# Kernel optimization log

Hardware: AMD Instinct MI355X
Metric: run time of the kernel (lower is better)

Reference implementation:

```python
import jax, jax.numpy as jnp
import numpy as np

B, S, D, VOCAB, K = 32, 128, 300, 20000, 8


def setup_inputs() -> dict:
    key = jax.random.key(0)
    ks = jax.random.split(key, 12)
    return {
        "words": jax.random.normal(ks[0], (B, S, D), jnp.float32),
        "lengths": jax.random.randint(ks[1], (B,), S // 2, S + 1),
        "vocab": jax.random.normal(ks[2], (VOCAB, D), jnp.float32) * 0.1,
        "default_embed": jax.random.uniform(ks[3], (D,), jnp.float32),
        "W": jnp.eye(D, dtype=jnp.float32) + 0.01 * jax.random.normal(ks[4], (D, D), jnp.float32),
        "lstm_Wih": jax.random.normal(ks[5], (4 * D, D), jnp.float32) * 0.05,
        "lstm_Whh": jax.random.normal(ks[6], (4 * D, D), jnp.float32) * 0.05,
        "lstm_bih": jnp.zeros((4 * D,), jnp.float32),
        "lstm_bhh": jnp.zeros((4 * D,), jnp.float32),
        "rnn_Wih": jax.random.normal(ks[7], (D, D), jnp.float32) * 0.05,
        "rnn_Whh": jax.random.normal(ks[8], (D, D), jnp.float32) * 0.05,
        "rnn_bih": jnp.zeros((D,), jnp.float32),
        "rnn_bhh": jnp.zeros((D,), jnp.float32),
    }


def _forward(words, lengths, vocab, default_embed, W,
             lstm_Wih, lstm_Whh, lstm_bih, lstm_bhh,
             rnn_Wih, rnn_Whh, rnn_bih, rnn_bhh):
    b, s, d = words.shape
    # --- NormalizeWordsModel (tagger) ---
    C = jnp.concatenate([vocab.T, default_embed[:, None]], axis=1)  # [D, V+1]
    P = jax.nn.softmax(jnp.einsum("bsd,de,ev->bsv", words, W, C), axis=-1)  # [B,S,V+1]
    V = P[..., -1:] * words + jnp.einsum("bsv,vd->bsd", P[..., :-1], vocab)  # [B,S,D]

    # --- LSTM encoder, final hidden at true length (packed-sequence semantics) ---
    valid = (jnp.arange(s)[None, :] < lengths[:, None])  # [B,S]

    def lstm_step(carry, xs):
        h, c = carry
        x_t, v_t = xs  # [B,D], [B]
        gates = x_t @ lstm_Wih.T + lstm_bih + h @ lstm_Whh.T + lstm_bhh  # [B,4D]
        i, f, g, o = jnp.split(gates, 4, axis=-1)
        c_new = jax.nn.sigmoid(f) * c + jax.nn.sigmoid(i) * jnp.tanh(g)
        h_new = jax.nn.sigmoid(o) * jnp.tanh(c_new)
        m = v_t[:, None]
        h = jnp.where(m, h_new, h)
        c = jnp.where(m, c_new, c)
        return (h, c), None

    h0 = jnp.zeros((b, d), V.dtype)
    (q, _), _ = jax.lax.scan(lstm_step, (h0, h0),
                             (jnp.swapaxes(V, 0, 1), valid.T))  # q: [B,D]

    # --- InstructionsDecoder: RNNCell applied K times to the same input q ---
    def rnn_step(h, _):
        h2 = jnp.tanh(q @ rnn_Wih.T + rnn_bih + h @ rnn_Whh.T + rnn_bhh)
        return h2, h2

    _, H = jax.lax.scan(rnn_step, h0, None, length=K)  # [K,B,D]
    H = jnp.swapaxes(H, 0, 1)  # [B,K,D]

    # --- masked softmax attention readout ---
    scores = jnp.einsum("bkd,bsd->bks", H, V)  # [B,K,S]
    scores = jnp.where(valid[:, None, :], scores, -jnp.inf)
    R = jnp.einsum("bks,bsd->bkd", jax.nn.softmax(scores, axis=-1), V)
    return R


def reference(words, lengths, vocab, default_embed, W,
              lstm_Wih, lstm_Whh, lstm_bih, lstm_bhh,
              rnn_Wih, rnn_Whh, rnn_bih, rnn_bhh):
    return _forward(words, lengths, vocab, default_embed, W,
                    lstm_Wih, lstm_Whh, lstm_bih, lstm_bhh,
                    rnn_Wih, rnn_Whh, rnn_bih, rnn_bhh)
```

## Files before the change

kernel.cpp:

```cpp
#include <hip/hip_runtime.h>


typedef unsigned short u16;
typedef unsigned int   u32;
typedef float  f32x4 __attribute__((ext_vector_type(4)));
typedef u32    u32x4 __attribute__((ext_vector_type(4)));
typedef __bf16 bf16x8 __attribute__((ext_vector_type(8)));
typedef _Float16 f16x2 __attribute__((ext_vector_type(2)));
typedef _Float16 f16x8 __attribute__((ext_vector_type(8)));

#define SCOPE_AGENT __HIP_MEMORY_SCOPE_AGENT

__device__ __forceinline__ float bf2f(u16 u) { return __uint_as_float(((u32)u) << 16); }
__device__ __forceinline__ u16 f2bf(float f) {
  u32 x = __float_as_uint(f);
  u32 r = (x + 0x7fffu + ((x >> 16) & 1u)) >> 16;
  return (u16)r;
}
__device__ __forceinline__ float sigm(float x) { return 1.f / (1.f + __expf(-x)); }
__device__ __forceinline__ u16 f2h(float f) {
  union { _Float16 h; u16 u; } cv; cv.h = (_Float16)f; return cv.u;
}
__device__ __forceinline__ float h2f(u16 u) {
  union { _Float16 h; u16 u; } cv; cv.u = u; return (float)cv.h;
}

__device__ __forceinline__ f32x4 shflx4(f32x4 v, int m) {
  f32x4 r;
  r[0] = __shfl_xor(v[0], m, 16);
  r[1] = __shfl_xor(v[1], m, 16);
  r[2] = __shfl_xor(v[2], m, 16);
  r[3] = __shfl_xor(v[3], m, 16);
  return r;
}

__device__ __forceinline__ void conv_seg(const void* src, u16* dst, int n, int is32,
                                         int t0, int stride) {
  if (is32) {
    const float* s = (const float*)src;
    for (int i = t0; i < n; i += stride) dst[i] = f2bf(s[i]);
  } else {
    const u16* s = (const u16*)src;
    for (int i = t0; i < n; i += stride) dst[i] = s[i];
  }
}

__global__ __launch_bounds__(256) void k_ingest(
    const void* words, const void* vocab, const void* de, const void* W,
    const void* lWih, const void* lWhh, const void* lbih, const void* lbhh,
    const void* rWih, const void* rWhh, const void* rbih, const void* rbhh,
    u16* cw, u16* cv, u16* cde, u16* cW, u16* cWih, u16* cWhh, u16* cbih, u16* cbhh,
    u16* crWih, u16* crWhh, u16* crbih, u16* crbhh, u32* flag, u32* seqz, u32* hbz) {
  __shared__ int s_is32;
  int tid = threadIdx.x;
  int vote = 0;
  if (tid < 64) {
    u32 w = ((const u32*)words)[tid];
    int e = (w >> 7) & 0xFF;
    vote = (e >= 100 && e <= 150) ? 1 : 0;
  }
  unsigned long long m = __ballot(vote);
  if (tid == 0) s_is32 = (__popcll(m) < 32) ? 1 : 0;
  __syncthreads();
  int is32 = s_is32;
  if (blockIdx.x == 0 && tid == 0) *flag = (u32)is32;
  int t0 = blockIdx.x * 256 + tid;
  int stride = gridDim.x * 256;
  if (t0 < 256) seqz[t0] = 0;
  if (t0 < 10240) hbz[t0] = 0;
  conv_seg(words, cw, 1228800, is32, t0, stride);
  conv_seg(vocab, cv, 6000000, is32, t0, stride);
  conv_seg(de, cde, 300, is32, t0, stride);
  conv_seg(W, cW, 90000, is32, t0, stride);
  conv_seg(lWih, cWih, 360000, is32, t0, stride);
  conv_seg(lWhh, cWhh, 360000, is32, t0, stride);
  conv_seg(lbih, cbih, 1200, is32, t0, stride);
  conv_seg(lbhh, cbhh, 1200, is32, t0, stride);
  conv_seg(rWih, crWih, 90000, is32, t0, stride);
  conv_seg(rWhh, crWhh, 90000, is32, t0, stride);
  conv_seg(rbih, crbih, 300, is32, t0, stride);
  conv_seg(rbhh, crbhh, 300, is32, t0, stride);
}

__global__ __launch_bounds__(256) void k_transpose_bf(const u16* __restrict__ in,
                                                      u16* __restrict__ out,
                                                      int J, int K) {
  __shared__ u16 t[32][33];
  int j0 = blockIdx.x * 32, k0 = blockIdx.y * 32;
  int lx = threadIdx.x & 31, ly = threadIdx.x >> 5;
  for (int r = ly; r < 32; r += 8) {
    int j = j0 + r, k = k0 + lx;
    t[r][lx] = (j < J && k < K) ? in[(size_t)j * K + k] : (u16)0;
  }
  __syncthreads();
  for (int r = ly; r < 32; r += 8) {
    int k = k0 + r, j = j0 + lx;
    if (k < K && j < J) out[(size_t)k * J + j] = t[lx][r];
  }
}

__global__ __launch_bounds__(256) void k_pack_w4(const u16* __restrict__ Whh,
                                                 u16* __restrict__ pW) {
  int idx = blockIdx.x * 256 + threadIdx.x;
  if (idx >= 16 * 25600) return;
  int bid = idx / 25600, r = idx % 25600;
  int t2 = r >> 9, lane = (r >> 3) & 63, j = r & 7;
  int nt = t2 / 10, kt = t2 % 10;
  int n = nt * 16 + (lane & 15);
  int gate = n / 20, dl = n % 20;
  int d0 = (bid < 15) ? 19 * bid : 285;
  int nd = (bid < 15) ? 19 : 15;
  int k = kt * 32 + ((lane >> 4) * 8) + j;
  u16 out = 0;
  if (dl < nd && k < 300) out = f2h(bf2f(Whh[(size_t)(gate * 300 + d0 + dl) * 300 + k]));
  pW[idx] = out;
}

__global__ __launch_bounds__(256) void k_pack_vocab(const u16* __restrict__ vocab,
                                                    u16* __restrict__ pA,
                                                    u16* __restrict__ pB) {
  __shared__ u16 sv[32][320];
  int ci = blockIdx.x, tid = threadIdx.x;
  for (int idx = tid; idx < 32 * 20; idx += 256) {
    int v = idx / 20, k = 300 + (idx - v * 20);
    sv[v][k] = 0;
  }
  for (int idx = tid; idx < 32 * 300; idx += 256) {
    int v = idx / 300, k = idx - v * 300;
    sv[v][k] = vocab[(size_t)(ci * 32 + v) * 300 + k];
  }
  __syncthreads();
  for (int idx = tid; idx < 10240; idx += 256) {
    int j = idx & 7, lane = (idx >> 3) & 63, t2 = idx >> 9;
    int kk = t2 % 10, h = t2 / 10;
    int v = h * 16 + (lane & 15);
    int k = kk * 32 + ((lane >> 4)) * 8 + j;
    pA[(size_t)ci * 10240 + (size_t)idx] = sv[v][k];
  }
  for (int idx = tid; idx < 9728; idx += 256) {
    int j = idx & 7, lane = (idx >> 3) & 63, nc = idx >> 9;
    int v = (lane >> 4) * 8 + j;
    int n = nc * 16 + (lane & 15);
    pB[(size_t)ci * 9728 + (size_t)idx] = sv[v][n];
  }
}

__global__ __launch_bounds__(256) void k_xw(const u16* __restrict__ words,
                                            const u16* __restrict__ W,
                                            u16* __restrict__ X) {
  __shared__ float As[300][33];
  int n0 = blockIdx.x * 128;
  int r0 = blockIdx.y * 32;
  int tid = threadIdx.x;
  for (int idx = tid; idx < 32 * 300; idx += 256) {
    int r = idx / 300, k = idx - r * 300;
    As[k][r] = bf2f(words[(size_t)(r0 + r) * 300 + k]);
  }
  __syncthreads();
  int j = n0 + (tid & 127);
  int rh = (tid >> 7) * 16;
  float acc[16];
#pragma unroll
  for (int i = 0; i < 16; i++) acc[i] = 0.f;
  if (j < 300) {
    for (int k = 0; k < 300; k++) {
      float bw = bf2f(W[(size_t)k * 300 + j]);
#pragma unroll
      for (int i = 0; i < 16; i++) acc[i] += As[k][rh + i] * bw;
    }
  }
  if (j < 320) {
#pragma unroll
    for (int i = 0; i < 16; i++) {
      float v = (j < 300) ? acc[i] : 0.f;
      X[(size_t)(r0 + rh + i) * 320 + j] = f2bf(v);
    }
  }
}

__global__ __launch_bounds__(512, 2) void k_softmax_v(
    const u16* __restrict__ X, const u16* __restrict__ pA, const u16* __restrict__ pB,
    u16* __restrict__ pAcc, float* __restrict__ pML) {
  __shared__ __align__(16) u16 chunk[19968];
  __shared__ __align__(16) float ptbuf[8 * 576];
  int bid = blockIdx.x;
  int sl = bid & 7, b = bid >> 3;
  int tid = threadIdx.x;
  int w = tid >> 6, lane = tid & 63;
  int quad = lane >> 4, n16 = lane & 15;
  int cs = (sl == 0) ? 0 : 79 + (sl - 1) * 78;
  int nch = (sl == 0) ? 79 : 78;

  int rowA = b * 128 + w * 16 + n16;
  const bf16x8* Xrow = (const bf16x8*)(X + (size_t)rowA * 320);
  bf16x8 afr[10];
#pragma unroll
  for (int kk = 0; kk < 10; kk++) afr[kk] = Xrow[kk * 4 + quad];

  f32x4 acc[19];
#pragma unroll
  for (int i = 0; i < 19; i++) { acc[i][0] = 0.f; acc[i][1] = 0.f; acc[i][2] = 0.f; acc[i][3] = 0.f; }
  f32x4 mrun, lrun;
#pragma unroll
  for (int c = 0; c < 4; c++) { mrun[c] = -1e30f; lrun[c] = 0.f; }
  float* myPt = ptbuf + w * 576;

  {
    const u32x4* gA = (const u32x4*)pA + (size_t)cs * 1280;
    const u32x4* gB = (const u32x4*)pB + (size_t)cs * 1216;
    u32x4* sb = (u32x4*)&chunk[0];
    for (int idx = tid; idx < 2496; idx += 512)
      sb[idx] = (idx < 1280) ? gA[idx] : gB[idx - 1280];
  }
  __syncthreads();

  for (int ic = 0; ic < nch; ic++) {
    u32x4 pf[5];
    bool havepf = (ic + 1 < nch);
    if (havepf) {
      int ci = cs + ic + 1;
      const u32x4* gA = (const u32x4*)pA + (size_t)ci * 1280;
      const u32x4* gB = (const u32x4*)pB + (size_t)ci * 1216;
#pragma unroll
      for (int i = 0; i < 5; i++) {
        int idx = tid + i * 512;
        if (idx < 2496) pf[i] = (idx < 1280) ? gA[idx] : gB[idx - 1280];
      }
    }
    const bf16x8* bufA = (const bf16x8*)&chunk[0];
    const bf16x8* bufB = (const bf16x8*)&chunk[10240];
    f32x4 L0, L1;
#pragma unroll
    for (int c = 0; c < 4; c++) { L0[c] = 0.f; L1[c] = 0.f; }
#pragma unroll
    for (int kk = 0; kk < 10; kk++) {
      L0 = __builtin_amdgcn_mfma_f32_16x16x32_bf16(afr[kk], bufA[kk * 64 + lane], L0, 0, 0, 0);
      L1 = __builtin_amdgcn_mfma_f32_16x16x32_bf16(afr[kk], bufA[(10 + kk) * 64 + lane], L1, 0, 0, 0);
    }
    f32x4 t;
#pragma unroll
    for (int c = 0; c < 4; c++) t[c] = fmaxf(L0[c], L1[c]);
#pragma unroll
    for (int off = 1; off < 16; off <<= 1) {
      f32x4 o = shflx4(t, off);
#pragma unroll
      for (int c = 0; c < 4; c++) t[c] = fmaxf(t[c], o[c]);
    }
    f32x4 mnew, al, P0v, P1v, rs;
#pragma unroll
    for (int c = 0; c < 4; c++) {
      mnew[c] = fmaxf(mrun[c], t[c]);
      al[c] = __expf(mrun[c] - mnew[c]);
      P0v[c] = __expf(L0[c] - mnew[c]);
      P1v[c] = __expf(L1[c] - mnew[c]);
      rs[c] = P0v[c] + P1v[c];
    }
#pragma unroll
    for (int off = 1; off < 16; off <<= 1) {
      f32x4 o = shflx4(rs, off);
#pragma unroll
      for (int c = 0; c < 4; c++) rs[c] += o[c];
    }
#pragma unroll
    for (int c = 0; c < 4; c++) { lrun[c] = lrun[c] * al[c] + rs[c]; mrun[c] = mnew[c]; }
#pragma unroll
    for (int r = 0; r < 4; r++) {
      myPt[(quad * 4 + r) * 36 + n16] = P0v[r];
      myPt[(quad * 4 + r) * 36 + 16 + n16] = P1v[r];
    }
    __syncthreads();
    f32x4 plo = *(const f32x4*)(myPt + n16 * 36 + quad * 8);
    f32x4 phi = *(const f32x4*)(myPt + n16 * 36 + quad * 8 + 4);
    bf16x8 paf;
#pragma unroll
    for (int c = 0; c < 4; c++) { paf[c] = (__bf16)plo[c]; paf[c + 4] = (__bf16)phi[c]; }
#pragma unroll
    for (int nc = 0; nc < 19; nc++) {
      f32x4 a = acc[nc];
#pragma unroll
      for (int c = 0; c < 4; c++) a[c] *= al[c];
      acc[nc] = __builtin_amdgcn_mfma_f32_16x16x32_bf16(paf, bufB[nc * 64 + lane], a, 0, 0, 0);
    }
    __syncthreads();
    if (havepf) {
      u32x4* sb = (u32x4*)&chunk[0];
#pragma unroll
      for (int i = 0; i < 5; i++) {
        int idx = tid + i * 512;
        if (idx < 2496) sb[idx] = pf[i];
      }
    }
    __syncthreads();
  }

  size_t prow = (size_t)sl * 4096 + (size_t)b * 128 + w * 16;
  if (n16 == 0) {
#pragma unroll
    for (int r = 0; r < 4; r++) {
      pML[(prow + quad * 4 + r) * 2 + 0] = mrun[r];
      pML[(prow + quad * 4 + r) * 2 + 1] = lrun[r];
    }
  }
#pragma unroll
  for (int nc = 0; nc < 19; nc++)
#pragma unroll
    for (int r = 0; r < 4; r++)
      pAcc[(prow + quad * 4 + r) * 304 + nc * 16 + n16] = f2bf(acc[nc][r]);
}

__global__ __launch_bounds__(320) void k_combine(
    const u16* __restrict__ pAcc, const float* __restrict__ pML,
    const u16* __restrict__ X, const u16* __restrict__ de,
    const u16* __restrict__ words, u16* __restrict__ Vout) {
  __shared__ float red[320];
  __shared__ float fs[8];
  __shared__ float sinv, sw;
  int row = blockIdx.x, tid = threadIdx.x;
  float p = 0.f;
  if (tid < 300) p = bf2f(X[(size_t)row * 320 + tid]) * bf2f(de[tid]);
  red[tid] = p;
  __syncthreads();
  if (tid == 0) {
    float d = 0.f;
    for (int i = 0; i < 300; i++) d += red[i];
    float mv[8], lv[8], ms = -1e30f;
    for (int s = 0; s < 8; s++) {
      mv[s] = pML[((size_t)s * 4096 + row) * 2];
      lv[s] = pML[((size_t)s * 4096 + row) * 2 + 1];
      ms = fmaxf(ms, mv[s]);
    }
    float mf = fmaxf(ms, d);
    float pd = __expf(d - mf);
    float l = pd;
    for (int s = 0; s < 8; s++) {
      float f = __expf(mv[s] - mf);
      fs[s] = f;
      l += lv[s] * f;
    }
    sinv = 1.f / l;
    sw = pd / l;
  }
  __syncthreads();
  float v = 0.f;
  if (tid < 300) {
    float a = 0.f;
#pragma unroll
    for (int s = 0; s < 8; s++)
      a += bf2f(pAcc[((size_t)s * 4096 + row) * 304 + tid]) * fs[s];
    v = a * sinv + sw * bf2f(words[(size_t)row * 300 + tid]);
  }
  Vout[(size_t)row * 320 + tid] = f2bf(v);
}

__global__ __launch_bounds__(256) void k_xg(const u16* __restrict__ Vb,
                                            const u16* __restrict__ WihT,
                                            const u16* __restrict__ bih,
                                            const u16* __restrict__ bhh,
                                            float* __restrict__ xg) {
  __shared__ float As[300][33];
  int n0 = blockIdx.x * 128;
  int r0 = blockIdx.y * 32;
  int tid = threadIdx.x;
  for (int idx = tid; idx < 32 * 300; idx += 256) {
    int r = idx / 300, k = idx - r * 300;
    As[k][r] = bf2f(Vb[(size_t)(r0 + r) * 320 + k]);
  }
  __syncthreads();
  int j = n0 + (tid & 127);
  if (j >= 1200) return;
  int rh = (tid >> 7) * 16;
  float acc[16];
#pragma unroll
  for (int i = 0; i < 16; i++) acc[i] = 0.f;
  for (int k = 0; k < 300; k++) {
    float bw = bf2f(WihT[(size_t)k * 1200 + j]);
#pragma unroll
    for (int i = 0; i < 16; i++) acc[i] += As[k][rh + i] * bw;
  }
  float bias = bf2f(bih[j]) + bf2f(bhh[j]);
#pragma unroll
  for (int i = 0; i < 16; i++)
    xg[(size_t)(r0 + rh + i) * 1200 + j] = acc[i] + bias;
}

__global__ __launch_bounds__(320, 1) void k_lstm2(
    const float* __restrict__ xg, const u16* __restrict__ pW,
    const int* __restrict__ lengths, u16* __restrict__ hb, u32* __restrict__ seq) {
  __shared__ float gl[32][84];
  __shared__ int s_maxlen;
  int bid = blockIdx.x, tid = threadIdx.x;
  int w = tid >> 6, lane = tid & 63;
  int quad = lane >> 4, n16 = lane & 15;
  int d0 = (bid < 15) ? 19 * bid : 285;
  int nd = (bid < 15) ? 19 : 15;
  {
    int lv = (tid < 32) ? lengths[tid] : 0;
    for (int off2 = 1; off2 < 32; off2 <<= 1) {
      int o = __shfl_xor(lv, off2, 64);
      lv = lv > o ? lv : o;
    }
    if (tid == 0) s_maxlen = lv;
  }
  f16x8 bf[10];
  const u32x4* pw4 = (const u32x4*)(pW + (size_t)bid * 25600);
#pragma unroll
  for (int kt = 0; kt < 10; kt++)
    bf[kt] = __builtin_bit_cast(f16x8, pw4[(w * 10 + kt) * 64 + lane]);
  int b0 = tid / 20, dl0 = tid - b0 * 20;
  int b1 = (tid + 320) / 20, dl1 = (tid + 320) - b1 * 20;
  bool a0 = dl0 < nd, a1 = dl1 < nd;
  int len0 = lengths[b0], len1 = lengths[b1];
  int dim0 = d0 + dl0, dim1 = d0 + dl1;
  int sa0 = (((b0 >> 4) * 10 + (dim0 >> 5)) * 64 + ((dim0 >> 3) & 3) * 16 + (b0 & 15)) * 8 + (dim0 & 7);
  int sa1 = (((b1 >> 4) * 10 + (dim1 >> 5)) * 64 + ((dim1 >> 3) & 3) * 16 + (b1 & 15)) * 8 + (dim1 & 7);
  float c0 = 0.f, h0 = 0.f, c1 = 0.f, h1 = 0.f;
  __syncthreads();
  int maxlen = s_maxlen;
  for (int t = 0; t < maxlen; t++) {
    if (tid < 16) {
      while (__hip_atomic_load(&seq[tid * 16], __ATOMIC_ACQUIRE, SCOPE_AGENT) < (u32)t)
        __builtin_amdgcn_s_sleep(2);
    }
    __syncthreads();
    float xv00 = 0.f, xv01 = 0.f, xv02 = 0.f, xv03 = 0.f;
    float xv10 = 0.f, xv11 = 0.f, xv12 = 0.f, xv13 = 0.f;
    const float* xr0 = xg + ((size_t)b0 * 128 + t) * 1200 + dim0;
    const float* xr1 = xg + ((size_t)b1 * 128 + t) * 1200 + dim1;
    if (a0) { xv00 = xr0[0]; xv01 = xr0[300]; xv02 = xr0[600]; xv03 = xr0[900]; }
    if (a1) { xv10 = xr1[0]; xv11 = xr1[300]; xv12 = xr1[600]; xv13 = xr1[900]; }
    const u32x4* hbt = (const u32x4*)hb + (size_t)(t & 1) * 1280;
    u32x4 af[2][10];
#pragma unroll
    for (int mt = 0; mt < 2; mt++)
#pragma unroll
      for (int kt = 0; kt < 10; kt++)
        af[mt][kt] = hbt[(mt * 10 + kt) * 64 + lane];
#pragma unroll
    for (int mt = 0; mt < 2; mt++) {
      f32x4 C;
      C[0] = 0.f; C[1] = 0.f; C[2] = 0.f; C[3] = 0.f;
#pragma unroll
      for (int kt = 0; kt < 10; kt++)
        C = __builtin_amdgcn_mfma_f32_16x16x32_f16(
            __builtin_bit_cast(f16x8, af[mt][kt]), bf[kt], C, 0, 0, 0);
#pragma unroll
      for (int rr = 0; rr < 4; rr++)
        gl[mt * 16 + quad * 4 + rr][w * 16 + n16] = C[rr];
    }
    __syncthreads();
    u16* hbw = hb + (size_t)((t + 1) & 1) * 10240;
    if (a0) {
      float gi = gl[b0][dl0] + xv00, gf = gl[b0][20 + dl0] + xv01;
      float gg = gl[b0][40 + dl0] + xv02, go = gl[b0][60 + dl0] + xv03;
      if (t < len0) {
        c0 = sigm(gf) * c0 + sigm(gi) * tanhf(gg);
        h0 = sigm(go) * tanhf(c0);
      }
      hbw[sa0] = f2h(h0);
    }
    if (a1) {
      float gi = gl[b1][dl1] + xv10, gf = gl[b1][20 + dl1] + xv11;
      float gg = gl[b1][40 + dl1] + xv12, go = gl[b1][60 + dl1] + xv13;
      if (t < len1) {
        c1 = sigm(gf) * c1 + sigm(gi) * tanhf(gg);
        h1 = sigm(go) * tanhf(c1);
      }
      hbw[sa1] = f2h(h1);
    }
    __syncthreads();
    if (tid == 0)
      __hip_atomic_store(&seq[bid * 16], (u32)(t + 1), __ATOMIC_RELEASE, SCOPE_AGENT);
  }
}

__global__ __launch_bounds__(320) void k_rnn(
    const u16* __restrict__ hb, const int* __restrict__ lengths,
    const u16* __restrict__ rWihT, const u16* __restrict__ rWhhT,
    const u16* __restrict__ rbih, const u16* __restrict__ rbhh,
    float* __restrict__ H) {
  __shared__ float qs[304], h2[304], base[304];
  __shared__ int s_maxlen;
  int b = blockIdx.x, tid = threadIdx.x;
  {
    int lv = (tid < 32) ? lengths[tid] : 0;
    for (int off2 = 1; off2 < 32; off2 <<= 1) {
      int o = __shfl_xor(lv, off2, 64);
      lv = lv > o ? lv : o;
    }
    if (tid == 0) s_maxlen = lv;
  }
  __syncthreads();
  int buf = s_maxlen & 1;
  if (tid < 304) {
    float q = 0.f;
    if (tid < 300) {
      int dim = tid;
      int idx = (((b >> 4) * 10 + (dim >> 5)) * 64 + ((dim >> 3) & 3) * 16 + (b & 15)) * 8 + (dim & 7);
      q = h2f(hb[(size_t)buf * 10240 + idx]);
    }
    qs[tid] = q;
    h2[tid] = 0.f;
  }
  __syncthreads();
  if (tid < 300) {
    float a = bf2f(rbih[tid]) + bf2f(rbhh[tid]);
    for (int k = 0; k < 300; k++) a += qs[k] * bf2f(rWihT[(size_t)k * 300 + tid]);
    base[tid] = a;
  }
  __syncthreads();
  for (int s = 0; s < 8; s++) {
    float nv = 0.f;
    if (tid < 300) {
      float a = base[tid];
      for (int k = 0; k < 300; k++) a += h2[k] * bf2f(rWhhT[(size_t)k * 300 + tid]);
      nv = tanhf(a);
    }
    __syncthreads();
    if (tid < 300) {
      h2[tid] = nv;
      H[((size_t)b * 8 + s) * 300 + tid] = nv;
    }
    __syncthreads();
  }
}

__global__ __launch_bounds__(256) void k_attn(const float* __restrict__ H,
                                              const u16* __restrict__ Vb,
                                              const int* __restrict__ lengths,
                                              const u32* __restrict__ flag,
                                              void* __restrict__ dout) {
  __shared__ float Hs[8][304];
  __shared__ float sc[8][128];
  __shared__ float wsum[8];
  int b = blockIdx.x, tid = threadIdx.x;
  int len = lengths[b];
  int is32 = (int)*flag;
  for (int idx = tid; idx < 8 * 300; idx += 256) {
    int k = idx / 300, j = idx - k * 300;
    Hs[k][j] = H[((size_t)b * 8 + k) * 300 + j];
  }
  __syncthreads();
  for (int s = tid; s < len; s += 256) {
    const u16* vr = Vb + (size_t)(b * 128 + s) * 320;
    float a[8];
#pragma unroll
    for (int k = 0; k < 8; k++) a[k] = 0.f;
    for (int j = 0; j < 300; j++) {
      float v = bf2f(vr[j]);
#pragma unroll
      for (int k = 0; k < 8; k++) a[k] += Hs[k][j] * v;
    }
#pragma unroll
    for (int k = 0; k < 8; k++) sc[k][s] = a[k];
  }
  __syncthreads();
  if (tid < 8) {
    float m = -1e30f;
    for (int s = 0; s < len; s++) m = fmaxf(m, sc[tid][s]);
    float l = 0.f;
    for (int s = 0; s < len; s++) { float e = __expf(sc[tid][s] - m); sc[tid][s] = e; l += e; }
    wsum[tid] = 1.f / l;
  }
  __syncthreads();
  int k = tid >> 5, jl = tid & 31;
  for (int j = jl; j < 300; j += 32) {
    float a = 0.f;
    for (int s = 0; s < len; s++) a += sc[k][s] * bf2f(Vb[(size_t)(b * 128 + s) * 320 + j]);
    float val = a * wsum[k];
    size_t o = ((size_t)b * 8 + k) * 300 + j;
    if (is32) ((float*)dout)[o] = val;
    else ((u16*)dout)[o] = f2bf(val);
  }
}

extern "C" void kernel_launch(void* const* d_in, const int* in_sizes, int n_in,
                              void* d_out, int out_size, void* d_ws, size_t ws_size,
                              hipStream_t stream) {
  (void)in_sizes; (void)n_in; (void)out_size; (void)ws_size;
  const void* words = d_in[0];
  const int* lengths = (const int*)d_in[1];
  const void* vocab = d_in[2];
  const void* de = d_in[3];
  const void* W = d_in[4];
  const void* lWih = d_in[5];
  const void* lWhh = d_in[6];
  const void* lbih = d_in[7];
  const void* lbhh = d_in[8];
  const void* rWih = d_in[9];
  const void* rWhh = d_in[10];
  const void* rbih = d_in[11];
  const void* rbhh = d_in[12];

  char* basep = (char*)d_ws;
  size_t off = 0;
  auto take = [&](size_t bytes) -> char* {
    char* p = basep + off;
    off += (bytes + 255) & ~(size_t)255;
    return p;
  };
  u16* cw    = (u16*)take(1228800 * 2);
  u16* cv    = (u16*)take(6000000 * 2);
  u16* cde   = (u16*)take(300 * 2);
  u16* cW    = (u16*)take(90000 * 2);
  u16* cWih  = (u16*)take(360000 * 2);
  u16* cWhh  = (u16*)take(360000 * 2);
  u16* cbih  = (u16*)take(1200 * 2);
  u16* cbhh  = (u16*)take(1200 * 2);
  u16* crWih = (u16*)take(90000 * 2);
  u16* crWhh = (u16*)take(90000 * 2);
  u16* crbih = (u16*)take(300 * 2);
  u16* crbhh = (u16*)take(300 * 2);
  u32* flag  = (u32*)take(256);
  u16*   X     = (u16*)take((size_t)4096 * 320 * 2);
  u16*   Vb    = (u16*)take((size_t)4096 * 320 * 2);
  u16*   WihT  = (u16*)take((size_t)300 * 1200 * 2);
  u16*   pW4   = (u16*)take((size_t)16 * 25600 * 2);
  u16*   rWihT = (u16*)take((size_t)300 * 300 * 2);
  u16*   rWhhT = (u16*)take((size_t)300 * 300 * 2);
  u16*   pAcc  = (u16*)take((size_t)8 * 4096 * 304 * 2);
  float* pML   = (float*)take((size_t)8 * 4096 * 2 * 4);
  float* H     = (float*)take((size_t)32 * 8 * 300 * 4);
  u16*   hb    = (u16*)take((size_t)2 * 10240 * 2);
  u32*   seq   = (u32*)take((size_t)4096 * 4);
  char* ureg = take((size_t)25000192);
  u16*   pA = (u16*)ureg;
  u16*   pB = (u16*)(ureg + (size_t)625 * 10240 * 2);
  float* xg = (float*)ureg;

  k_ingest<<<4096, 256, 0, stream>>>(words, vocab, de, W, lWih, lWhh, lbih, lbhh,
                                     rWih, rWhh, rbih, rbhh,
                                     cw, cv, cde, cW, cWih, cWhh, cbih, cbhh,
                                     crWih, crWhh, crbih, crbhh, flag, seq, (u32*)hb);
  k_transpose_bf<<<dim3(38, 10), 256, 0, stream>>>(cWih, WihT, 1200, 300);
  k_transpose_bf<<<dim3(10, 10), 256, 0, stream>>>(crWih, rWihT, 300, 300);
  k_transpose_bf<<<dim3(10, 10), 256, 0, stream>>>(crWhh, rWhhT, 300, 300);
  k_pack_w4<<<1600, 256, 0, stream>>>(cWhh, pW4);
  k_pack_vocab<<<625, 256, 0, stream>>>(cv, pA, pB);
  k_xw<<<dim3(3, 128), 256, 0, stream>>>(cw, cW, X);
  k_softmax_v<<<256, 512, 0, stream>>>(X, pA, pB, pAcc, pML);
  k_combine<<<4096, 320, 0, stream>>>(pAcc, pML, X, cde, cw, Vb);
  k_xg<<<dim3(10, 128), 256, 0, stream>>>(Vb, WihT, cbih, cbhh, xg);
  k_lstm2<<<16, 320, 0, stream>>>(xg, pW4, lengths, hb, seq);
  k_rnn<<<32, 320, 0, stream>>>(hb, lengths, rWihT, rWhhT, crbih, crbhh, H);
  k_attn<<<32, 256, 0, stream>>>(H, Vb, lengths, flag, d_out);
}
```

Before: 1.082 ms.

## Restructure LSTM recurrence into 19 single-wave blocks with register-resident weights

Replaces the 16-block, 320-thread LSTM kernel with 19 active single-wavefront blocks. Each block owns 16 hidden dims across all four gates and keeps its Whh fragments in registers. The gate math is done directly from MFMA accumulators, which removes the shared-memory gate staging and the per-step __syncthreads barriers. The input projection is now written as fp16 in a lane-packed layout, so each lane loads its step's inputs with four vector loads, and a new pad kernel zeroes the unused tail. The risks are lower precision for the input gates, busy-spin flag polling without sleep, and launching 152 blocks of which only every eighth does work, presumably to spread the active ones across CUs.

```diff
diff --git a/kernel.cpp b/kernel.cpp
--- a/kernel.cpp
+++ b/kernel.cpp
@@ -66,8 +66,8 @@
   if (blockIdx.x == 0 && tid == 0) *flag = (u32)is32;
   int t0 = blockIdx.x * 256 + tid;
   int stride = gridDim.x * 256;
-  if (t0 < 256) seqz[t0] = 0;
-  if (t0 < 10240) hbz[t0] = 0;
+  if (t0 < 608) seqz[t0] = 0;
+  if (t0 < 40960) hbz[t0] = 0;
   conv_seg(words, cw, 1228800, is32, t0, stride);
   conv_seg(vocab, cv, 6000000, is32, t0, stride);
   conv_seg(de, cde, 300, is32, t0, stride);
@@ -99,21 +99,19 @@
   }
 }
 
-__global__ __launch_bounds__(256) void k_pack_w4(const u16* __restrict__ Whh,
-                                                 u16* __restrict__ pW) {
+__global__ __launch_bounds__(256) void k_pack_wA(const u16* __restrict__ Whh,
+                                                 u16* __restrict__ pWn) {
   int idx = blockIdx.x * 256 + threadIdx.x;
-  if (idx >= 16 * 25600) return;
-  int bid = idx / 25600, r = idx % 25600;
-  int t2 = r >> 9, lane = (r >> 3) & 63, j = r & 7;
-  int nt = t2 / 10, kt = t2 % 10;
-  int n = nt * 16 + (lane & 15);
-  int gate = n / 20, dl = n % 20;
-  int d0 = (bid < 15) ? 19 * bid : 285;
-  int nd = (bid < 15) ? 19 : 15;
+  if (idx >= 389120) return;
+  int j = idx & 7, lane = (idx >> 3) & 63;
+  int t2 = idx >> 9;
+  int kt = t2 % 10, gw = t2 / 10;
+  int gate = gw & 3, wid = gw >> 2;
+  int dim = wid * 16 + (lane & 15);
   int k = kt * 32 + ((lane >> 4) * 8) + j;
   u16 out = 0;
-  if (dl < nd && k < 300) out = f2h(bf2f(Whh[(size_t)(gate * 300 + d0 + dl) * 300 + k]));
-  pW[idx] = out;
+  if (dim < 300 && k < 300) out = f2h(bf2f(Whh[(size_t)(gate * 300 + dim) * 300 + k]));
+  pWn[idx] = out;
 }
 
 __global__ __launch_bounds__(256) void k_pack_vocab(const u16* __restrict__ vocab,
@@ -352,11 +350,18 @@
   Vout[(size_t)row * 320 + tid] = f2bf(v);
 }
 
+__global__ __launch_bounds__(256) void k_xgp_pad(u32* __restrict__ xgp) {
+  int i = blockIdx.x * 256 + threadIdx.x;
+  if (i >= 32768) return;
+  int t = i >> 8, lane = 48 + ((i >> 4) & 15), d = i & 15;
+  xgp[((size_t)(t * 19 + 18) * 64 + lane) * 16 + d] = 0;
+}
+
 __global__ __launch_bounds__(256) void k_xg(const u16* __restrict__ Vb,
                                             const u16* __restrict__ WihT,
                                             const u16* __restrict__ bih,
                                             const u16* __restrict__ bhh,
-                                            float* __restrict__ xg) {
+                                            u16* __restrict__ xgp) {
   __shared__ float As[300][33];
   int n0 = blockIdx.x * 128;
   int r0 = blockIdx.y * 32;
@@ -378,98 +383,101 @@
     for (int i = 0; i < 16; i++) acc[i] += As[k][rh + i] * bw;
   }
   float bias = bf2f(bih[j]) + bf2f(bhh[j]);
-#pragma unroll
-  for (int i = 0; i < 16; i++)
-    xg[(size_t)(r0 + rh + i) * 1200 + j] = acc[i] + bias;
-}
-
-__global__ __launch_bounds__(320, 1) void k_lstm2(
-    const float* __restrict__ xg, const u16* __restrict__ pW,
+  int gate = j / 300, dim = j - gate * 300;
+  int wid = dim >> 4, dl = dim & 15;
+  int qd = dl >> 2, reg = dl & 3, rp = reg >> 1, half = reg & 1;
+  int b = r0 >> 7;
+  int tb = (r0 & 127) + rh;
+  size_t lanepart = (size_t)(qd * 16 + (b & 15)) * 16 + (b >> 4) * 8 + gate * 2 + rp;
+#pragma unroll
+  for (int i = 0; i < 16; i++) {
+    size_t u32idx = ((size_t)((tb + i) * 19 + wid) * 64) * 16 + lanepart;
+    xgp[u32idx * 2 + half] = f2h(acc[i] + bias);
+  }
+}
+
+__global__ __launch_bounds__(64, 1) void k_lstm3(
+    const u16* __restrict__ xgp, const u16* __restrict__ pWn,
     const int* __restrict__ lengths, u16* __restrict__ hb, u32* __restrict__ seq) {
-  __shared__ float gl[32][84];
-  __shared__ int s_maxlen;
-  int bid = blockIdx.x, tid = threadIdx.x;
-  int w = tid >> 6, lane = tid & 63;
+  int bid = blockIdx.x;
+  if (bid & 7) return;
+  int wid = bid >> 3;
+  if (wid >= 19) return;
+  int lane = threadIdx.x;
   int quad = lane >> 4, n16 = lane & 15;
-  int d0 = (bid < 15) ? 19 * bid : 285;
-  int nd = (bid < 15) ? 19 : 15;
-  {
-    int lv = (tid < 32) ? lengths[tid] : 0;
-    for (int off2 = 1; off2 < 32; off2 <<= 1) {
-      int o = __shfl_xor(lv, off2, 64);
-      lv = lv > o ? lv : o;
-    }
-    if (tid == 0) s_maxlen = lv;
-  }
-  f16x8 bf[10];
-  const u32x4* pw4 = (const u32x4*)(pW + (size_t)bid * 25600);
-#pragma unroll
-  for (int kt = 0; kt < 10; kt++)
-    bf[kt] = __builtin_bit_cast(f16x8, pw4[(w * 10 + kt) * 64 + lane]);
-  int b0 = tid / 20, dl0 = tid - b0 * 20;
-  int b1 = (tid + 320) / 20, dl1 = (tid + 320) - b1 * 20;
-  bool a0 = dl0 < nd, a1 = dl1 < nd;
-  int len0 = lengths[b0], len1 = lengths[b1];
-  int dim0 = d0 + dl0, dim1 = d0 + dl1;
-  int sa0 = (((b0 >> 4) * 10 + (dim0 >> 5)) * 64 + ((dim0 >> 3) & 3) * 16 + (b0 & 15)) * 8 + (dim0 & 7);
-  int sa1 = (((b1 >> 4) * 10 + (dim1 >> 5)) * 64 + ((dim1 >> 3) & 3) * 16 + (b1 & 15)) * 8 + (dim1 & 7);
-  float c0 = 0.f, h0 = 0.f, c1 = 0.f, h1 = 0.f;
-  __syncthreads();
-  int maxlen = s_maxlen;
+  int lv = (lane < 32) ? lengths[lane] : 0;
+#pragma unroll
+  for (int o = 1; o < 64; o <<= 1) {
+    int x = __shfl_xor(lv, o, 64);
+    lv = lv > x ? lv : x;
+  }
+  int maxlen = lv;
+  int len0 = lengths[n16], len1 = lengths[16 + n16];
+  u32x4 afr[4][10];
+  const u32x4* pw = (const u32x4*)pWn + (size_t)wid * 40 * 64;
+#pragma unroll
+  for (int g = 0; g < 4; g++)
+#pragma unroll
+    for (int kt = 0; kt < 10; kt++)
+      afr[g][kt] = pw[(g * 10 + kt) * 64 + lane];
+  float cst[2][4], hst[2][4];
+#pragma unroll
+  for (int mt = 0; mt < 2; mt++)
+#pragma unroll
+    for (int r = 0; r < 4; r++) { cst[mt][r] = 0.f; hst[mt][r] = 0.f; }
+
   for (int t = 0; t < maxlen; t++) {
-    if (tid < 16) {
-      while (__hip_atomic_load(&seq[tid * 16], __ATOMIC_ACQUIRE, SCOPE_AGENT) < (u32)t)
-        __builtin_amdgcn_s_sleep(2);
-    }
-    __syncthreads();
-    float xv00 = 0.f, xv01 = 0.f, xv02 = 0.f, xv03 = 0.f;
-    float xv10 = 0.f, xv11 = 0.f, xv12 = 0.f, xv13 = 0.f;
-    const float* xr0 = xg + ((size_t)b0 * 128 + t) * 1200 + dim0;
-    const float* xr1 = xg + ((size_t)b1 * 128 + t) * 1200 + dim1;
-    if (a0) { xv00 = xr0[0]; xv01 = xr0[300]; xv02 = xr0[600]; xv03 = xr0[900]; }
-    if (a1) { xv10 = xr1[0]; xv11 = xr1[300]; xv12 = xr1[600]; xv13 = xr1[900]; }
-    const u32x4* hbt = (const u32x4*)hb + (size_t)(t & 1) * 1280;
-    u32x4 af[2][10];
-#pragma unroll
-    for (int mt = 0; mt < 2; mt++)
+    u32 Xd[16];
+    {
+      const u32x4* xb = (const u32x4*)xgp + ((size_t)(t * 19 + wid) * 64 + lane) * 4;
+      *(u32x4*)&Xd[0] = xb[0];
+      *(u32x4*)&Xd[4] = xb[1];
+      *(u32x4*)&Xd[8] = xb[2];
+      *(u32x4*)&Xd[12] = xb[3];
+    }
+    if (lane < 19) {
+      while (__hip_atomic_load(&seq[lane * 32], __ATOMIC_ACQUIRE, SCOPE_AGENT) < (u32)t) {}
+    }
+    int rbuf = t & 1, wbuf = rbuf ^ 1;
+    const u16* hbr = hb + (size_t)rbuf * 40960;
+#pragma unroll
+    for (int mt = 0; mt < 2; mt++) {
+      int batch = mt * 16 + n16;
+      const u16* hbase = hbr + batch * 1280 + (quad & 1) * 8;
+      u32x4 bfr[10];
 #pragma unroll
       for (int kt = 0; kt < 10; kt++)
-        af[mt][kt] = hbt[(mt * 10 + kt) * 64 + lane];
-#pragma unroll
-    for (int mt = 0; mt < 2; mt++) {
-      f32x4 C;
-      C[0] = 0.f; C[1] = 0.f; C[2] = 0.f; C[3] = 0.f;
+        bfr[kt] = *(const u32x4*)(hbase + (kt * 2 + (quad >> 1)) * 64);
+      f32x4 C[4];
+#pragma unroll
+      for (int g = 0; g < 4; g++) { C[g][0] = 0.f; C[g][1] = 0.f; C[g][2] = 0.f; C[g][3] = 0.f; }
 #pragma unroll
       for (int kt = 0; kt < 10; kt++)
-        C = __builtin_amdgcn_mfma_f32_16x16x32_f16(
-            __builtin_bit_cast(f16x8, af[mt][kt]), bf[kt], C, 0, 0, 0);
-#pragma unroll
-      for (int rr = 0; rr < 4; rr++)
-        gl[mt * 16 + quad * 4 + rr][w * 16 + n16] = C[rr];
-    }
-    __syncthreads();
-    u16* hbw = hb + (size_t)((t + 1) & 1) * 10240;
-    if (a0) {
-      float gi = gl[b0][dl0] + xv00, gf = gl[b0][20 + dl0] + xv01;
-      float gg = gl[b0][40 + dl0] + xv02, go = gl[b0][60 + dl0] + xv03;
-      if (t < len0) {
-        c0 = sigm(gf) * c0 + sigm(gi) * tanhf(gg);
-        h0 = sigm(go) * tanhf(c0);
+#pragma unroll
+        for (int g = 0; g < 4; g++)
+          C[g] = __builtin_amdgcn_mfma_f32_16x16x32_f16(
+              __builtin_bit_cast(f16x8, afr[g][kt]),
+              __builtin_bit_cast(f16x8, bfr[kt]), C[g], 0, 0, 0);
+      int lenm = mt ? len1 : len0;
+      bool upd = t < lenm;
+#pragma unroll
+      for (int reg = 0; reg < 4; reg++) {
+        int rp = reg >> 1, hf = (reg & 1) * 16;
+        float gi = h2f((u16)(Xd[mt * 8 + 0 + rp] >> hf)) + C[0][reg];
+        float gf = h2f((u16)(Xd[mt * 8 + 2 + rp] >> hf)) + C[1][reg];
+        float gg = h2f((u16)(Xd[mt * 8 + 4 + rp] >> hf)) + C[2][reg];
+        float go = h2f((u16)(Xd[mt * 8 + 6 + rp] >> hf)) + C[3][reg];
+        float cc = sigm(gf) * cst[mt][reg] + sigm(gi) * tanhf(gg);
+        float hv = sigm(go) * tanhf(cc);
+        cst[mt][reg] = upd ? cc : cst[mt][reg];
+        hst[mt][reg] = upd ? hv : hst[mt][reg];
       }
-      hbw[sa0] = f2h(h0);
-    }
-    if (a1) {
-      float gi = gl[b1][dl1] + xv10, gf = gl[b1][20 + dl1] + xv11;
-      float gg = gl[b1][40 + dl1] + xv12, go = gl[b1][60 + dl1] + xv13;
-      if (t < len1) {
-        c1 = sigm(gf) * c1 + sigm(gi) * tanhf(gg);
-        h1 = sigm(go) * tanhf(c1);
-      }
-      hbw[sa1] = f2h(h1);
-    }
-    __syncthreads();
-    if (tid == 0)
-      __hip_atomic_store(&seq[bid * 16], (u32)(t + 1), __ATOMIC_RELEASE, SCOPE_AGENT);
+      u32* hw = (u32*)hb + (size_t)wbuf * 20480 + batch * 640 + wid * 32 + quad * 2;
+      hw[0] = (u32)f2h(hst[mt][0]) | ((u32)f2h(hst[mt][1]) << 16);
+      hw[1] = (u32)f2h(hst[mt][2]) | ((u32)f2h(hst[mt][3]) << 16);
+    }
+    if (lane == 0)
+      __hip_atomic_store(&seq[wid * 32], (u32)(t + 1), __ATOMIC_RELEASE, SCOPE_AGENT);
   }
 }
 
@@ -483,9 +491,9 @@
   int b = blockIdx.x, tid = threadIdx.x;
   {
     int lv = (tid < 32) ? lengths[tid] : 0;
-    for (int off2 = 1; off2 < 32; off2 <<= 1) {
-      int o = __shfl_xor(lv, off2, 64);
-      lv = lv > o ? lv : o;
+    for (int o = 1; o < 64; o <<= 1) {
+      int x = __shfl_xor(lv, o, 64);
+      lv = lv > x ? lv : x;
     }
     if (tid == 0) s_maxlen = lv;
   }
@@ -495,8 +503,7 @@
     float q = 0.f;
     if (tid < 300) {
       int dim = tid;
-      int idx = (((b >> 4) * 10 + (dim >> 5)) * 64 + ((dim >> 3) & 3) * 16 + (b & 15)) * 8 + (dim & 7);
-      q = h2f(hb[(size_t)buf * 10240 + idx]);
+      q = h2f(hb[(size_t)buf * 40960 + b * 1280 + (dim >> 4) * 64 + (dim & 15)]);
     }
     qs[tid] = q;
     h2[tid] = 0.f;
@@ -614,18 +621,18 @@
   u16*   X     = (u16*)take((size_t)4096 * 320 * 2);
   u16*   Vb    = (u16*)take((size_t)4096 * 320 * 2);
   u16*   WihT  = (u16*)take((size_t)300 * 1200 * 2);
-  u16*   pW4   = (u16*)take((size_t)16 * 25600 * 2);
+  u16*   pWn   = (u16*)take((size_t)389120 * 2);
   u16*   rWihT = (u16*)take((size_t)300 * 300 * 2);
   u16*   rWhhT = (u16*)take((size_t)300 * 300 * 2);
   u16*   pAcc  = (u16*)take((size_t)8 * 4096 * 304 * 2);
   float* pML   = (float*)take((size_t)8 * 4096 * 2 * 4);
   float* H     = (float*)take((size_t)32 * 8 * 300 * 4);
-  u16*   hb    = (u16*)take((size_t)2 * 10240 * 2);
+  u16*   hb    = (u16*)take((size_t)2 * 40960 * 2);
   u32*   seq   = (u32*)take((size_t)4096 * 4);
   char* ureg = take((size_t)25000192);
-  u16*   pA = (u16*)ureg;
-  u16*   pB = (u16*)(ureg + (size_t)625 * 10240 * 2);
-  float* xg = (float*)ureg;
+  u16*   pA  = (u16*)ureg;
+  u16*   pB  = (u16*)(ureg + (size_t)625 * 10240 * 2);
+  u16*   xgp = (u16*)ureg;
 
   k_ingest<<<4096, 256, 0, stream>>>(words, vocab, de, W, lWih, lWhh, lbih, lbhh,
                                      rWih, rWhh, rbih, rbhh,
@@ -634,13 +641,14 @@
   k_transpose_bf<<<dim3(38, 10), 256, 0, stream>>>(cWih, WihT, 1200, 300);
   k_transpose_bf<<<dim3(10, 10), 256, 0, stream>>>(crWih, rWihT, 300, 300);
   k_transpose_bf<<<dim3(10, 10), 256, 0, stream>>>(crWhh, rWhhT, 300, 300);
-  k_pack_w4<<<1600, 256, 0, stream>>>(cWhh, pW4);
+  k_pack_wA<<<1520, 256, 0, stream>>>(cWhh, pWn);
   k_pack_vocab<<<625, 256, 0, stream>>>(cv, pA, pB);
   k_xw<<<dim3(3, 128), 256, 0, stream>>>(cw, cW, X);
   k_softmax_v<<<256, 512, 0, stream>>>(X, pA, pB, pAcc, pML);
   k_combine<<<4096, 320, 0, stream>>>(pAcc, pML, X, cde, cw, Vb);
-  k_xg<<<dim3(10, 128), 256, 0, stream>>>(Vb, WihT, cbih, cbhh, xg);
-  k_lstm2<<<16, 320, 0, stream>>>(xg, pW4, lengths, hb, seq);
+  k_xgp_pad<<<128, 256, 0, stream>>>((u32*)xgp);
+  k_xg<<<dim3(10, 128), 256, 0, stream>>>(Vb, WihT, cbih, cbhh, xgp);
+  k_lstm3<<<152, 64, 0, stream>>>(xgp, pWn, lengths, hb, seq);
   k_rnn<<<32, 320, 0, stream>>>(hb, lengths, rWihT, rWhhT, crbih, crbhh, H);
   k_attn<<<32, 256, 0, stream>>>(H, Vb, lengths, flag, d_out);
 }
```

After: 1.703 ms. 57.4% more time.
